# Performance work log

Hardware: AMD Instinct MI355X
Metric: run time of the kernel (lower is better)

Reference implementation:

```python
import jax, jax.numpy as jnp
import numpy as np

B, N, F, D, K = 128, 512, 64, 64, 20  # batch, nodes, input_dim, dim, topk


def setup_inputs() -> dict:
    key = jax.random.key(0)
    ks = jax.random.split(key, 9)
    s = 1.0 / np.sqrt(D)
    return dict(
        data=jax.random.normal(ks[0], (B, N, F), jnp.float32),
        org_edge_index=jax.random.randint(ks[1], (2, 1024), 0, N),
        embed=jax.random.normal(ks[2], (N, D), jnp.float32),
        W_lin=jax.random.normal(ks[3], (F, D), jnp.float32) / np.sqrt(F),
        att_i=jax.random.normal(ks[4], (D,), jnp.float32) * s,
        att_j=jax.random.normal(ks[5], (D,), jnp.float32) * s,
        att_em_i=jax.random.normal(ks[6], (D,), jnp.float32) * s,
        att_em_j=jax.random.normal(ks[7], (D,), jnp.float32) * s,
        gnn_bias=jnp.zeros((D,), jnp.float32),
        bn1_gamma=jnp.ones((D,), jnp.float32),
        bn1_beta=jnp.zeros((D,), jnp.float32),
        bn2_gamma=jnp.ones((D,), jnp.float32),
        bn2_beta=jnp.zeros((D,), jnp.float32),
        out_W=jax.random.normal(ks[8], (D, 1), jnp.float32) * s,
        out_b=jnp.zeros((1,), jnp.float32),
    )


def reference(data, embed, W_lin, att_i, att_j, att_em_i, att_em_j, gnn_bias,
              bn1_gamma, bn1_beta, bn2_gamma, bn2_beta, out_W, out_b,
              org_edge_index):
    eps = 1e-5
    slope = 0.2  # LeakyReLU negative slope (PyG GATConv default)
    BN_ = B * N

    # Encoder -> learned graph: cosine similarity + topk (GDN-style)
    e_norm = embed / (jnp.linalg.norm(embed, axis=-1, keepdims=True) + 1e-12)
    weight_arr = e_norm @ e_norm.T                      # [N, N]
    _, topk_idx = jax.lax.top_k(weight_arr, K)          # [N, K]

    src = topk_idx.reshape(-1)                          # gated_j (message source)
    dst = jnp.repeat(jnp.arange(N), K)                  # gated_i (message dest)
    self_mask = src == dst                              # remove_self_loops

    # batched edge index (block-diagonal over batch)
    offs = (jnp.arange(B) * N)[:, None]
    src_b = (src[None, :] + offs).reshape(-1)
    dst_b = (dst[None, :] + offs).reshape(-1)
    mask_b = jnp.tile(self_mask, B)

    # add_self_loops for all B*N nodes
    loops = jnp.arange(BN_)
    src_all = jnp.concatenate([src_b, loops])
    dst_all = jnp.concatenate([dst_b, loops])
    mask_all = jnp.concatenate([mask_b, jnp.zeros((BN_,), bool)])

    # GraphLayer: linear transform + embedding-augmented attention
    x = data.reshape(BN_, F)
    g = x @ W_lin                                       # [BN, D]
    emb_all = jnp.tile(embed, (B, 1))                   # [BN, D]
    s_i = g @ att_i + emb_all @ att_em_i                # per-node dest score
    s_j = g @ att_j + emb_all @ att_em_j                # per-node src score
    logits = jax.nn.leaky_relu(s_i[dst_all] + s_j[src_all], slope)
    logits = jnp.where(mask_all, -jnp.inf, logits)      # removed self edges

    # softmax over incoming edges of each destination node
    m = jax.ops.segment_max(logits, dst_all, num_segments=BN_)
    ex = jnp.exp(logits - m[dst_all])
    denom = jax.ops.segment_sum(ex, dst_all, num_segments=BN_)
    attn = ex / denom[dst_all]

    agg = jax.ops.segment_sum(g[src_all] * attn[:, None], dst_all,
                              num_segments=BN_) + gnn_bias  # [BN, D]

    # BatchNorm1d (batch stats) + ReLU
    mu = agg.mean(0)
    var = agg.var(0)
    h = jax.nn.relu((agg - mu) / jnp.sqrt(var + eps) * bn1_gamma + bn1_beta)

    # multiply by node embedding, channel BN over (batch, node), ReLU
    h = h.reshape(B, N, D) * embed[None]
    mu2 = h.mean(axis=(0, 1))
    var2 = h.var(axis=(0, 1))
    h = jax.nn.relu((h - mu2) / jnp.sqrt(var2 + eps) * bn2_gamma + bn2_beta)

    # OutLayer (layer_num=1): Linear(D, 1)
    out = (h @ out_W + out_b).reshape(B, N)
    return out
```

## Files before the change

### kernel.cpp

```cpp
#include <hip/hip_runtime.h>
#include <math.h>

#define Bsz 128
#define Nn  512
#define Fd  64
#define Dd  64
#define Kk  20
#define BN  (Bsz*Nn)
#define NCPY 16
#define ET_STRIDE 129
#define SMEM_BYTES (64*ET_STRIDE*4 + 256*4)

__device__ __forceinline__ float wave_sum64(float v){
  #pragma unroll
  for (int o = 32; o; o >>= 1) v += __shfl_xor(v, o, 64);
  return v;
}
__device__ __forceinline__ float wave_max64(float v){
  #pragma unroll
  for (int o = 32; o; o >>= 1) v = fmaxf(v, __shfl_xor(v, o, 64));
  return v;
}
__device__ __forceinline__ float leaky(float v){ return (v >= 0.f) ? v : 0.2f*v; }

__device__ __forceinline__ int wave_argmax_idx(float v, int idx){
  int vi = __float_as_int(v);
#define DPP_STEP(CTRL) { \
    int nv = __builtin_amdgcn_update_dpp(vi,  vi,  CTRL, 0xF, 0xF, false); \
    int ni = __builtin_amdgcn_update_dpp(idx, idx, CTRL, 0xF, 0xF, false); \
    float fnv = __int_as_float(nv), fov = __int_as_float(vi); \
    bool take = (fnv > fov) || ((fnv == fov) && (ni < idx)); \
    vi = take ? nv : vi; idx = take ? ni : idx; \
  }
  DPP_STEP(0x111)
  DPP_STEP(0x112)
  DPP_STEP(0x114)
  DPP_STEP(0x118)
  DPP_STEP(0x142)
  DPP_STEP(0x143)
#undef DPP_STEP
  return __builtin_amdgcn_readlane(idx, 63);
}

__global__ __launch_bounds__(256) void k1(const float* __restrict__ x,
    const float* __restrict__ W, const float* __restrict__ embed,
    const float* __restrict__ att_i, const float* __restrict__ att_j,
    const float* __restrict__ aem_i, const float* __restrict__ aem_j,
    float* __restrict__ g, float* __restrict__ s_i, float* __restrict__ s_j,
    int* __restrict__ topk){
  __shared__ __align__(16) char smem[SMEM_BYTES];
  int tid = threadIdx.x, b = blockIdx.x;

  if (b >= 128){
    int bl = b - 128;
    float4* sW   = (float4*)smem;
    float4* sai  = (float4*)(smem + 16384);
    float4* saj  = sai + 16;
    float4* semi = saj + 16;
    float4* semj = semi + 16;
    const float4* W4 = (const float4*)W;
    #pragma unroll
    for (int t = 0; t < 4; t++) sW[tid + 256*t] = W4[tid + 256*t];
    if (tid < 16){
      sai[tid]  = ((const float4*)att_i)[tid];
      saj[tid]  = ((const float4*)att_j)[tid];
      semi[tid] = ((const float4*)aem_i)[tid];
      semj[tid] = ((const float4*)aem_j)[tid];
    }
    __syncthreads();
    int rowgrp = tid >> 4, cg = tid & 15;
    int row0 = bl*64 + rowgrp*4;
    float4 acc0={0,0,0,0}, acc1={0,0,0,0}, acc2={0,0,0,0}, acc3={0,0,0,0};
    const float4* xr0 = (const float4*)(x + (row0+0)*Fd);
    const float4* xr1 = (const float4*)(x + (row0+1)*Fd);
    const float4* xr2 = (const float4*)(x + (row0+2)*Fd);
    const float4* xr3 = (const float4*)(x + (row0+3)*Fd);
    for (int qk = 0; qk < 16; qk++){
      float4 x0 = xr0[qk], x1 = xr1[qk], x2 = xr2[qk], x3 = xr3[qk];
      float xs0[4] = {x0.x,x0.y,x0.z,x0.w};
      float xs1[4] = {x1.x,x1.y,x1.z,x1.w};
      float xs2[4] = {x2.x,x2.y,x2.z,x2.w};
      float xs3[4] = {x3.x,x3.y,x3.z,x3.w};
      #pragma unroll
      for (int s = 0; s < 4; s++){
        float4 w4 = sW[(4*qk + s)*16 + cg];
        acc0.x += xs0[s]*w4.x; acc0.y += xs0[s]*w4.y; acc0.z += xs0[s]*w4.z; acc0.w += xs0[s]*w4.w;
        acc1.x += xs1[s]*w4.x; acc1.y += xs1[s]*w4.y; acc1.z += xs1[s]*w4.z; acc1.w += xs1[s]*w4.w;
        acc2.x += xs2[s]*w4.x; acc2.y += xs2[s]*w4.y; acc2.z += xs2[s]*w4.z; acc2.w += xs2[s]*w4.w;
        acc3.x += xs3[s]*w4.x; acc3.y += xs3[s]*w4.y; acc3.z += xs3[s]*w4.z; acc3.w += xs3[s]*w4.w;
      }
    }
    float4 ai = sai[cg], aj = saj[cg], emi = semi[cg], emj = semj[cg];
    float4 avv[4] = {acc0, acc1, acc2, acc3};
    #pragma unroll
    for (int r = 0; r < 4; r++){
      int row = row0 + r;
      int node = row & (Nn-1);
      float4 a4 = avv[r];
      float4 e4 = ((const float4*)embed)[node*16 + cg];
      float si = a4.x*ai.x + a4.y*ai.y + a4.z*ai.z + a4.w*ai.w
               + e4.x*emi.x + e4.y*emi.y + e4.z*emi.z + e4.w*emi.w;
      float sj = a4.x*aj.x + a4.y*aj.y + a4.z*aj.z + a4.w*aj.w
               + e4.x*emj.x + e4.y*emj.y + e4.z*emj.z + e4.w*emj.w;
      #pragma unroll
      for (int o = 1; o < 16; o <<= 1){
        si += __shfl_xor(si, o, 64);
        sj += __shfl_xor(sj, o, 64);
      }
      if (cg == 0){ s_i[row] = si; s_j[row] = sj; }
      ((float4*)(g + row*Dd))[cg] = a4;
    }
  } else {
    int bb = b;
    float* eT = (float*)smem;
    float* se = (float*)(smem + 64*ET_STRIDE*4);
    int wv = tid >> 6, lane = tid & 63;
    se[tid] = embed[bb*256 + tid];
    const float4* emb4 = (const float4*)embed;
    float av[8];
    #pragma unroll
    for (int tt = 0; tt < 4; tt++){
      float4 stg[8];
      #pragma unroll
      for (int j = 0; j < 8; j++)
        stg[j] = emb4[tt*2048 + j*256 + tid];
      __syncthreads();
      #pragma unroll
      for (int j = 0; j < 8; j++){
        float4 v = stg[j];
        float ss = v.x*v.x + v.y*v.y + v.z*v.z + v.w*v.w;
        #pragma unroll
        for (int o = 1; o < 16; o <<= 1) ss += __shfl_xor(ss, o, 64);
        float rn = 1.f/(sqrtf(ss) + 1e-12f);
        int row_local = j*16 + (tid >> 4);
        int d0 = (tid & 15)*4;
        eT[(d0+0)*ET_STRIDE + row_local] = v.x*rn;
        eT[(d0+1)*ET_STRIDE + row_local] = v.y*rn;
        eT[(d0+2)*ET_STRIDE + row_local] = v.z*rn;
        eT[(d0+3)*ET_STRIDE + row_local] = v.w*rn;
      }
      __syncthreads();
      const float4* sef4 = (const float4*)(se + wv*64);
      float a0 = 0.f, a1 = 0.f;
      #pragma unroll
      for (int d4 = 0; d4 < 16; d4++){
        float4 q4 = sef4[d4];
        int d = d4*4;
        a0 += q4.x*eT[(d+0)*ET_STRIDE + lane] + q4.y*eT[(d+1)*ET_STRIDE + lane]
            + q4.z*eT[(d+2)*ET_STRIDE + lane] + q4.w*eT[(d+3)*ET_STRIDE + lane];
        a1 += q4.x*eT[(d+0)*ET_STRIDE + 64 + lane] + q4.y*eT[(d+1)*ET_STRIDE + 64 + lane]
            + q4.z*eT[(d+2)*ET_STRIDE + 64 + lane] + q4.w*eT[(d+3)*ET_STRIDE + 64 + lane];
      }
      av[2*tt]   = a0;
      av[2*tt+1] = a1;
    }
    int row = bb*4 + wv;
    #pragma unroll 1
    for (int t = 0; t < Kk; t++){
      float bv = av[0]; int br = 0;
      #pragma unroll
      for (int rep = 1; rep < 8; rep++)
        if (av[rep] > bv){ bv = av[rep]; br = rep; }
      int ci = br*64 + lane;
      int win = wave_argmax_idx(bv, ci);
      if (lane == 0) topk[row*Kk + t] = win;
      int wr = win >> 6;
      if ((win & 63) == lane){
        #pragma unroll
        for (int rep = 0; rep < 8; rep++)
          if (rep == wr) av[rep] = -INFINITY;
      }
    }
  }
}

__global__ __launch_bounds__(256) void k2(const float* __restrict__ g,
    const float* __restrict__ s_i, const float* __restrict__ s_j,
    const int* __restrict__ topk, const float* __restrict__ bias,
    float* __restrict__ agg, float* __restrict__ stats){
  __shared__ float  swt[4][4][24];
  __shared__ int    sji[4][4][24];
  __shared__ float4 sred_s[4][16], sred_q[4][16];
  __shared__ float4 sbias[16];
  int tid = threadIdx.x, wv = tid >> 6, lane = tid & 63;
  if (tid < 16) sbias[tid] = ((const float4*)bias)[tid];
  __syncthreads();
  int bid = blockIdx.x;
  int xcd = bid & 7, q = bid >> 3;
  int batch = xcd*16 + (q & 15);
  int quarter = q >> 4;
  int base = batch*Nn;
  int node0 = quarter*128 + wv*32;
  const float4* g4 = (const float4*)g;
  int h = lane >> 4, c = lane & 15;
  float4 s4 = {0,0,0,0}, q4 = {0,0,0,0};
  #pragma unroll 1
  for (int gI = 0; gI < 8; gI++){
    #pragma unroll
    for (int h4 = 0; h4 < 4; h4++){
      int node = node0 + gI*4 + h4;
      int dest = base + node;
      float si_d = s_i[dest];
      float lg = -INFINITY; int j = node;
      if (lane < Kk){
        j = topk[node*Kk + lane];
        if (j != node) lg = leaky(si_d + s_j[base + j]);
      } else if (lane == Kk){
        lg = leaky(si_d + s_j[dest]);
      }
      float m  = wave_max64(lg);
      float e_ = (lane <= Kk) ? __expf(lg - m) : 0.f;
      float denom = wave_sum64(e_);
      if (lane < 24){
        swt[wv][h4][lane] = (lane <= Kk) ? e_/denom : 0.f;
        sji[wv][h4][lane] = j;
      }
    }
    float la[24]; int ja[24];
    const float4* lv = (const float4*)swt[wv][h];
    const int4*   jv = (const int4*)sji[wv][h];
    #pragma unroll
    for (int qq = 0; qq < 6; qq++){
      float4 f = lv[qq]; la[4*qq]=f.x; la[4*qq+1]=f.y; la[4*qq+2]=f.z; la[4*qq+3]=f.w;
      int4  ii = jv[qq]; ja[4*qq]=ii.x; ja[4*qq+1]=ii.y; ja[4*qq+2]=ii.z; ja[4*qq+3]=ii.w;
    }
    float4 acc = sbias[c];
    #pragma unroll
    for (int e = 0; e <= Kk; e++){
      float4 gv = g4[(base + ja[e])*16 + c];
      acc.x += la[e]*gv.x; acc.y += la[e]*gv.y; acc.z += la[e]*gv.z; acc.w += la[e]*gv.w;
    }
    int dest = base + node0 + gI*4 + h;
    ((float4*)agg)[dest*16 + c] = acc;
    s4.x += acc.x; s4.y += acc.y; s4.z += acc.z; s4.w += acc.w;
    q4.x += acc.x*acc.x; q4.y += acc.y*acc.y; q4.z += acc.z*acc.z; q4.w += acc.w*acc.w;
  }
  #pragma unroll
  for (int o = 16; o <= 32; o <<= 1){
    s4.x += __shfl_xor(s4.x,o,64); s4.y += __shfl_xor(s4.y,o,64);
    s4.z += __shfl_xor(s4.z,o,64); s4.w += __shfl_xor(s4.w,o,64);
    q4.x += __shfl_xor(q4.x,o,64); q4.y += __shfl_xor(q4.y,o,64);
    q4.z += __shfl_xor(q4.z,o,64); q4.w += __shfl_xor(q4.w,o,64);
  }
  if (lane < 16){ sred_s[wv][lane] = s4; sred_q[wv][lane] = q4; }
  __syncthreads();
  float* sc = stats + (bid & (NCPY-1))*256;
  if (wv == 0 && lane < 16){
    float4 a = sred_s[0][lane];
    #pragma unroll
    for (int w = 1; w < 4; w++){ float4 t = sred_s[w][lane]; a.x+=t.x; a.y+=t.y; a.z+=t.z; a.w+=t.w; }
    atomicAdd(&sc[lane*4+0], a.x); atomicAdd(&sc[lane*4+1], a.y);
    atomicAdd(&sc[lane*4+2], a.z); atomicAdd(&sc[lane*4+3], a.w);
  }
  if (wv == 1 && lane < 16){
    float4 a = sred_q[0][lane];
    #pragma unroll
    for (int w = 1; w < 4; w++){ float4 t = sred_q[w][lane]; a.x+=t.x; a.y+=t.y; a.z+=t.z; a.w+=t.w; }
    atomicAdd(&sc[64+lane*4+0], a.x); atomicAdd(&sc[64+lane*4+1], a.y);
    atomicAdd(&sc[64+lane*4+2], a.z); atomicAdd(&sc[64+lane*4+3], a.w);
  }
}

__global__ __launch_bounds__(256) void k3(const float* __restrict__ agg,
    const float* __restrict__ embed, const float* __restrict__ bn1g,
    const float* __restrict__ bn1b, float* __restrict__ stats){
  __shared__ float ssc[64], ssh[64];
  __shared__ float4 sred_s[4][16], sred_q[4][16];
  int tid = threadIdx.x;
  if (tid < 64){
    float s = 0.f, qq = 0.f;
    #pragma unroll
    for (int x = 0; x < NCPY; x++){ s += stats[x*256 + tid]; qq += stats[x*256 + 64 + tid]; }
    float mu = s*(1.f/BN), var = qq*(1.f/BN) - mu*mu;
    float sc = bn1g[tid]/sqrtf(var + 1e-5f);
    ssc[tid] = sc; ssh[tid] = bn1b[tid] - mu*sc;
  }
  __syncthreads();
  int gt = blockIdx.x*256 + tid;
  int c = gt & 15, r0 = gt >> 4;
  int wv = tid >> 6, lane = tid & 63;
  float4 sc1 = ((const float4*)ssc)[c], sh1 = ((const float4*)ssh)[c];
  float4 e4 = ((const float4*)embed)[(r0 & (Nn-1))*16 + c];
  float4 s4 = {0,0,0,0}, q4 = {0,0,0,0};
  const float4* a4 = (const float4*)agg;
  for (int r = r0; r < BN; r += 4096){
    float4 v = a4[r*16 + c];
    v.x = fmaxf(v.x*sc1.x+sh1.x, 0.f)*e4.x;
    v.y = fmaxf(v.y*sc1.y+sh1.y, 0.f)*e4.y;
    v.z = fmaxf(v.z*sc1.z+sh1.z, 0.f)*e4.z;
    v.w = fmaxf(v.w*sc1.w+sh1.w, 0.f)*e4.w;
    s4.x += v.x; s4.y += v.y; s4.z += v.z; s4.w += v.w;
    q4.x += v.x*v.x; q4.y += v.y*v.y; q4.z += v.z*v.z; q4.w += v.w*v.w;
  }
  #pragma unroll
  for (int o = 16; o <= 32; o <<= 1){
    s4.x += __shfl_xor(s4.x,o,64); s4.y += __shfl_xor(s4.y,o,64);
    s4.z += __shfl_xor(s4.z,o,64); s4.w += __shfl_xor(s4.w,o,64);
    q4.x += __shfl_xor(q4.x,o,64); q4.y += __shfl_xor(q4.y,o,64);
    q4.z += __shfl_xor(q4.z,o,64); q4.w += __shfl_xor(q4.w,o,64);
  }
  if (lane < 16){ sred_s[wv][lane] = s4; sred_q[wv][lane] = q4; }
  __syncthreads();
  float* sc = stats + (blockIdx.x & (NCPY-1))*256;
  if (wv == 0 && lane < 16){
    float4 a = sred_s[0][lane];
    #pragma unroll
    for (int w = 1; w < 4; w++){ float4 t = sred_s[w][lane]; a.x+=t.x; a.y+=t.y; a.z+=t.z; a.w+=t.w; }
    atomicAdd(&sc[128+lane*4+0], a.x); atomicAdd(&sc[128+lane*4+1], a.y);
    atomicAdd(&sc[128+lane*4+2], a.z); atomicAdd(&sc[128+lane*4+3], a.w);
  }
  if (wv == 1 && lane < 16){
    float4 a = sred_q[0][lane];
    #pragma unroll
    for (int w = 1; w < 4; w++){ float4 t = sred_q[w][lane]; a.x+=t.x; a.y+=t.y; a.z+=t.z; a.w+=t.w; }
    atomicAdd(&sc[192+lane*4+0], a.x); atomicAdd(&sc[192+lane*4+1], a.y);
    atomicAdd(&sc[192+lane*4+2], a.z); atomicAdd(&sc[192+lane*4+3], a.w);
  }
}

__global__ __launch_bounds__(256) void k4(const float* __restrict__ agg,
    const float* __restrict__ embed, const float* __restrict__ bn1g,
    const float* __restrict__ bn1b, const float* __restrict__ bn2g,
    const float* __restrict__ bn2b, const float* __restrict__ outW,
    const float* __restrict__ outb, const float* __restrict__ stats,
    float* __restrict__ out){
  __shared__ float ssc1[64], ssh1[64], ssc2[64], ssh2[64];
  int tid = threadIdx.x;
  if (tid < 64){
    float s1=0.f, q1=0.f, s2=0.f, q2=0.f;
    #pragma unroll
    for (int x = 0; x < NCPY; x++){
      const float* p = stats + x*256;
      s1 += p[tid]; q1 += p[64+tid]; s2 += p[128+tid]; q2 += p[192+tid];
    }
    float mu1 = s1*(1.f/BN), var1 = q1*(1.f/BN) - mu1*mu1;
    float sc1 = bn1g[tid]/sqrtf(var1 + 1e-5f);
    ssc1[tid] = sc1; ssh1[tid] = bn1b[tid] - mu1*sc1;
    float mu2 = s2*(1.f/BN), var2 = q2*(1.f/BN) - mu2*mu2;
    float sc2 = bn2g[tid]/sqrtf(var2 + 1e-5f);
    ssc2[tid] = sc2; ssh2[tid] = bn2b[tid] - mu2*sc2;
  }
  __syncthreads();
  int gt = blockIdx.x*256 + tid;
  int c = gt & 15, r0 = gt >> 4;
  float4 sc1 = ((const float4*)ssc1)[c], sh1 = ((const float4*)ssh1)[c];
  float4 sc2 = ((const float4*)ssc2)[c], sh2 = ((const float4*)ssh2)[c];
  float4 ow  = ((const float4*)outW)[c];
  float ob = outb[0];
  float4 e4 = ((const float4*)embed)[(r0 & (Nn-1))*16 + c];
  const float4* a4 = (const float4*)agg;
  for (int r = r0; r < BN; r += 4096){
    float4 v = a4[r*16 + c];
    v.x = fmaxf(v.x*sc1.x+sh1.x, 0.f)*e4.x;
    v.y = fmaxf(v.y*sc1.y+sh1.y, 0.f)*e4.y;
    v.z = fmaxf(v.z*sc1.z+sh1.z, 0.f)*e4.z;
    v.w = fmaxf(v.w*sc1.w+sh1.w, 0.f)*e4.w;
    float t = fmaxf(v.x*sc2.x+sh2.x, 0.f)*ow.x
            + fmaxf(v.y*sc2.y+sh2.y, 0.f)*ow.y
            + fmaxf(v.z*sc2.z+sh2.z, 0.f)*ow.z
            + fmaxf(v.w*sc2.w+sh2.w, 0.f)*ow.w;
    #pragma unroll
    for (int o = 1; o < 16; o <<= 1) t += __shfl_xor(t, o, 64);
    if (c == 0) out[r] = t + ob;
  }
}

extern "C" void kernel_launch(void* const* d_in, const int* in_sizes, int n_in,
                              void* d_out, int out_size, void* d_ws, size_t ws_size,
                              hipStream_t stream){
  const float* data  = (const float*)d_in[0];
  const float* embed = (const float*)d_in[2];
  const float* W_lin = (const float*)d_in[3];
  const float* att_i = (const float*)d_in[4];
  const float* att_j = (const float*)d_in[5];
  const float* aem_i = (const float*)d_in[6];
  const float* aem_j = (const float*)d_in[7];
  const float* bias  = (const float*)d_in[8];
  const float* g1    = (const float*)d_in[9];
  const float* b1    = (const float*)d_in[10];
  const float* g2    = (const float*)d_in[11];
  const float* b2    = (const float*)d_in[12];
  const float* outW  = (const float*)d_in[13];
  const float* outb  = (const float*)d_in[14];
  float* out = (float*)d_out;

  float* ws    = (float*)d_ws;
  float* g     = ws;
  float* agg   = ws + 4194304;
  float* s_i   = ws + 8388608;
  float* s_j   = s_i + 65536;
  int*   topk  = (int*)(s_j + 65536);
  float* stats = (float*)(topk + Nn*Kk);

  hipMemsetAsync(stats, 0, NCPY*256*sizeof(float), stream);
  k1<<<1152, 256, 0, stream>>>(data, W_lin, embed, att_i, att_j, aem_i, aem_j,
                               g, s_i, s_j, topk);
  k2<<<512, 256, 0, stream>>>(g, s_i, s_j, topk, bias, agg, stats);
  k3<<<256, 256, 0, stream>>>(agg, embed, g1, b1, stats);
  k4<<<256, 256, 0, stream>>>(agg, embed, g1, b1, g2, b2, outW, outb, stats, out);
}
```

Measured before the change: 169.0 us.

## Split softmax across half-waves and launch more blocks for k2-k4

The attention softmax in k2 now handles two destination nodes per wave, one per 32-lane half, using half-wave shuffle reductions. This halves the shuffle and exp work per node. Each k2 block covers fewer nodes, so the grid grows to 2048 blocks, and k3/k4 also launch 2048 blocks with a larger row stride. The stats copy count doubles to spread atomic contention. More blocks raise occupancy and parallelism, at the cost of more per-block setup and more stats partials to reduce.

```diff
diff --git a/kernel.cpp b/kernel.cpp
--- a/kernel.cpp
+++ b/kernel.cpp
@@ -7,20 +7,10 @@
 #define Dd  64
 #define Kk  20
 #define BN  (Bsz*Nn)
-#define NCPY 16
+#define NCPY 32
 #define ET_STRIDE 129
 #define SMEM_BYTES (64*ET_STRIDE*4 + 256*4)
 
-__device__ __forceinline__ float wave_sum64(float v){
-  #pragma unroll
-  for (int o = 32; o; o >>= 1) v += __shfl_xor(v, o, 64);
-  return v;
-}
-__device__ __forceinline__ float wave_max64(float v){
-  #pragma unroll
-  for (int o = 32; o; o >>= 1) v = fmaxf(v, __shfl_xor(v, o, 64));
-  return v;
-}
 __device__ __forceinline__ float leaky(float v){ return (v >= 0.f) ? v : 0.2f*v; }
 
 __device__ __forceinline__ int wave_argmax_idx(float v, int idx){
@@ -188,32 +178,37 @@
   int bid = blockIdx.x;
   int xcd = bid & 7, q = bid >> 3;
   int batch = xcd*16 + (q & 15);
-  int quarter = q >> 4;
+  int six = q >> 4;
   int base = batch*Nn;
-  int node0 = quarter*128 + wv*32;
+  int node0 = six*32 + wv*8;
   const float4* g4 = (const float4*)g;
   int h = lane >> 4, c = lane & 15;
+  int half = lane >> 5, ln = lane & 31;
   float4 s4 = {0,0,0,0}, q4 = {0,0,0,0};
   #pragma unroll 1
-  for (int gI = 0; gI < 8; gI++){
-    #pragma unroll
-    for (int h4 = 0; h4 < 4; h4++){
-      int node = node0 + gI*4 + h4;
+  for (int gI = 0; gI < 2; gI++){
+    #pragma unroll
+    for (int pr = 0; pr < 2; pr++){
+      int node = node0 + gI*4 + pr*2 + half;
       int dest = base + node;
       float si_d = s_i[dest];
       float lg = -INFINITY; int j = node;
-      if (lane < Kk){
-        j = topk[node*Kk + lane];
+      if (ln < Kk){
+        j = topk[node*Kk + ln];
         if (j != node) lg = leaky(si_d + s_j[base + j]);
-      } else if (lane == Kk){
+      } else if (ln == Kk){
         lg = leaky(si_d + s_j[dest]);
       }
-      float m  = wave_max64(lg);
-      float e_ = (lane <= Kk) ? __expf(lg - m) : 0.f;
-      float denom = wave_sum64(e_);
-      if (lane < 24){
-        swt[wv][h4][lane] = (lane <= Kk) ? e_/denom : 0.f;
-        sji[wv][h4][lane] = j;
+      float m = lg;
+      #pragma unroll
+      for (int o = 16; o; o >>= 1) m = fmaxf(m, __shfl_xor(m, o, 64));
+      float e_ = (ln <= Kk) ? __expf(lg - m) : 0.f;
+      float denom = e_;
+      #pragma unroll
+      for (int o = 16; o; o >>= 1) denom += __shfl_xor(denom, o, 64);
+      if (ln < 24){
+        swt[wv][pr*2+half][ln] = (ln <= Kk) ? e_/denom : 0.f;
+        sji[wv][pr*2+half][ln] = j;
       }
     }
     float la[24]; int ja[24];
@@ -283,7 +278,7 @@
   float4 e4 = ((const float4*)embed)[(r0 & (Nn-1))*16 + c];
   float4 s4 = {0,0,0,0}, q4 = {0,0,0,0};
   const float4* a4 = (const float4*)agg;
-  for (int r = r0; r < BN; r += 4096){
+  for (int r = r0; r < BN; r += 32768){
     float4 v = a4[r*16 + c];
     v.x = fmaxf(v.x*sc1.x+sh1.x, 0.f)*e4.x;
     v.y = fmaxf(v.y*sc1.y+sh1.y, 0.f)*e4.y;
@@ -349,7 +344,7 @@
   float ob = outb[0];
   float4 e4 = ((const float4*)embed)[(r0 & (Nn-1))*16 + c];
   const float4* a4 = (const float4*)agg;
-  for (int r = r0; r < BN; r += 4096){
+  for (int r = r0; r < BN; r += 32768){
     float4 v = a4[r*16 + c];
     v.x = fmaxf(v.x*sc1.x+sh1.x, 0.f)*e4.x;
     v.y = fmaxf(v.y*sc1.y+sh1.y, 0.f)*e4.y;
@@ -395,7 +390,7 @@
   hipMemsetAsync(stats, 0, NCPY*256*sizeof(float), stream);
   k1<<<1152, 256, 0, stream>>>(data, W_lin, embed, att_i, att_j, aem_i, aem_j,
                                g, s_i, s_j, topk);
-  k2<<<512, 256, 0, stream>>>(g, s_i, s_j, topk, bias, agg, stats);
-  k3<<<256, 256, 0, stream>>>(agg, embed, g1, b1, stats);
-  k4<<<256, 256, 0, stream>>>(agg, embed, g1, b1, g2, b2, outW, outb, stats, out);
-}
+  k2<<<2048, 256, 0, stream>>>(g, s_i, s_j, topk, bias, agg, stats);
+  k3<<<2048, 256, 0, stream>>>(agg, embed, g1, b1, stats);
+  k4<<<2048, 256, 0, stream>>>(agg, embed, g1, b1, g2, b2, outW, outb, stats, out);
+}
```

New measurement: 151.8 us. 1.11x faster.
